# Kernel optimization log

Measured on AMD Instinct MI355X. Metric: run time of the kernel, lower is better.

## Reference

```python
import jax, jax.numpy as jnp
import numpy as np

C = 256
DEPTH = 4
GRIDS = [(128, 128), (128, 128), (128, 128)]
B = 2
N = 32768


def _ln_c(x, g, b):
    # LayerNorm over channel dim of [B, C, N] (myLayerNorm transposes to [B,N,C])
    m = x.mean(axis=1, keepdims=True)
    v = ((x - m) ** 2).mean(axis=1, keepdims=True)
    return (x - m) * jax.lax.rsqrt(v + 1e-5) * g[None, :, None] + b[None, :, None]


def _bn_train(x, g, b):
    # BatchNorm1d (training-mode batch stats) over [B, C, L]
    m = x.mean(axis=(0, 2), keepdims=True)
    v = ((x - m) ** 2).mean(axis=(0, 2), keepdims=True)
    return (x - m) * jax.lax.rsqrt(v + 1e-5) * g[None, :, None] + b[None, :, None]


def _dwconv3(x, w, b):
    # depthwise 3x3 conv, SAME padding; x [B,C,H,W], w [C,3,3]
    out = jax.lax.conv_general_dilated(x, w[:, None, :, :], (1, 1), 'SAME',
                                       feature_group_count=C,
                                       dimension_numbers=('NCHW', 'OIHW', 'NCHW'))
    return out + b[None, :, None, None]


def setup_inputs() -> dict:
    key = jax.random.key(0)
    ks = jax.random.split(key, 20)
    tokens = jax.random.normal(ks[0], (B, C, N), jnp.float32)
    hw = GRIDS[0][0] * GRIDS[0][1]
    cell_ind = jax.random.randint(ks[1], (B, 3, N), 0, hw)
    occupied_cell = jnp.ones((B, N), jnp.float32)

    def p(k, shape, scale=0.05):
        return scale * jax.random.normal(k, shape, jnp.float32)

    inp = dict(tokens=tokens, cell_ind=cell_ind, occupied_cell=occupied_cell)
    inp['smix_ln_g'] = 1.0 + p(ks[2], (DEPTH, C))
    inp['smix_ln_b'] = p(ks[3], (DEPTH, C))
    inp['ffn_w1'] = p(ks[4], (DEPTH, C, 3, 3), 0.2)
    inp['ffn_b1'] = p(ks[5], (DEPTH, C))
    inp['ffn_w2'] = p(ks[6], (DEPTH, C, 3, 3), 0.2)
    inp['ffn_b2'] = p(ks[7], (DEPTH, C))
    inp['att_scale'] = 1.0 + p(ks[8], (DEPTH, C))
    inp['att_bn_g'] = 1.0 + p(ks[9], (DEPTH, C))
    inp['att_bn_b'] = p(ks[10], (DEPTH, C))
    inp['cmix_ln_g'] = 1.0 + p(ks[11], (DEPTH, C))
    inp['cmix_ln_b'] = p(ks[12], (DEPTH, C))
    inp['cmix_w1'] = p(ks[13], (DEPTH, C, C), 1.0 / float(np.sqrt(C)))
    inp['cmix_b1'] = p(ks[14], (DEPTH, C))
    inp['cmix_w2'] = p(ks[15], (DEPTH, C, C), 1.0 / float(np.sqrt(C)))
    inp['cmix_b2'] = p(ks[16], (DEPTH, C))
    inp['cmix_scale'] = p(ks[17], (DEPTH, C), 0.1)
    return inp


def _forward(tokens, occupied_cell, cell_ind,
             smix_ln_g, smix_ln_b, ffn_w1, ffn_b1, ffn_w2, ffn_b2,
             att_scale, att_bn_g, att_bn_b,
             cmix_ln_g, cmix_ln_b, cmix_w1, cmix_b1, cmix_w2, cmix_b2, cmix_scale):
    Bx, Cx, Nx = tokens.shape
    bidx = jnp.arange(Bx)[:, None]
    # build_proj_matrix equivalent: per-point 1/(points-in-cell) weights + clamped indices
    sp = []
    for g in range(len(GRIDS)):
        HW = GRIDS[g][0] * GRIDS[g][1]
        ci = jnp.clip(cell_ind[:, g], 0, HW - 1)
        # inflate^T @ occupied: per-cell occupied count (occupied^2 per point)
        counts = jnp.zeros((Bx, HW), tokens.dtype).at[bidx, ci].add(occupied_cell * occupied_cell)
        # inflate @ counts: per-point count of points sharing its cell
        npp = occupied_cell * jnp.take_along_axis(counts, ci, axis=1)
        sp.append((ci, occupied_cell / (npp + 1e-6)))
    skip = [jnp.zeros(GRIDS[g], tokens.dtype) for g in range(len(GRIDS))]
    for d in range(DEPTH):
        g = d % len(GRIDS)
        H, W = GRIDS[g]
        HW = H * W
        ci, wpt = sp[g]
        # --- SpatialMix ---
        r = _ln_c(tokens, smix_ln_g[d], smix_ln_b[d]) * wpt[:, None, :]
        grid = jnp.zeros((Bx, Cx, HW), tokens.dtype).at[
            jnp.arange(Bx)[:, None, None], jnp.arange(Cx)[None, :, None], ci[:, None, :]].add(r)
        grid = grid.reshape(Bx, Cx, H, W) + skip[g]
        plane = _dwconv3(jax.nn.relu(_dwconv3(grid, ffn_w1[d], ffn_b1[d])), ffn_w2[d], ffn_b2[d])
        rflat = plane.reshape(Bx, Cx, HW)
        att = jax.nn.sigmoid(_bn_train(rflat * att_scale[d][None, :, None], att_bn_g[d], att_bn_b[d]))
        rflat = att * rflat
        r = jnp.take_along_axis(rflat, jnp.broadcast_to(ci[:, None, :], (Bx, Cx, Nx)), axis=2)
        tokens = tokens + r
        skip[g] = plane
        # --- ChannelMix ---
        h = _ln_c(tokens, cmix_ln_g[d], cmix_ln_b[d])
        h = jnp.einsum('oc,bcn->bon', cmix_w1[d], h) + cmix_b1[d][None, :, None]
        h = jnp.einsum('oc,bcn->bon', cmix_w2[d], jax.nn.relu(h)) + cmix_b2[d][None, :, None]
        tokens = tokens + h * cmix_scale[d][None, :, None]
    return tokens


def reference(tokens, cell_ind, occupied_cell,
              smix_ln_g, smix_ln_b, ffn_w1, ffn_b1, ffn_w2, ffn_b2,
              att_scale, att_bn_g, att_bn_b,
              cmix_ln_g, cmix_ln_b, cmix_w1, cmix_b1, cmix_w2, cmix_b2, cmix_scale):
    return _forward(tokens, occupied_cell, cell_ind,
                    smix_ln_g, smix_ln_b, ffn_w1, ffn_b1, ffn_w2, ffn_b2,
                    att_scale, att_bn_g, att_bn_b,
                    cmix_ln_g, cmix_ln_b, cmix_w1, cmix_b1, cmix_w2, cmix_b2, cmix_scale)
```

## Files before the change

kernel.cpp:

```cpp
#include <hip/hip_runtime.h>
#include <hip/hip_bf16.h>
#include <hip/hip_fp16.h>

#define Cc 256
#define Nn 32768
#define HWc 16384
#define Bb 2

typedef float floatx4 __attribute__((ext_vector_type(4)));
typedef short bf16x8 __attribute__((ext_vector_type(8)));
typedef unsigned short ushort8v __attribute__((ext_vector_type(8)));
typedef unsigned short ushort4v __attribute__((ext_vector_type(4)));

__device__ __forceinline__ unsigned short f2b(float f){
    unsigned u = __float_as_uint(f);
    u += 0x7fff + ((u >> 16) & 1);
    return (unsigned short)(u >> 16);
}
__device__ __forceinline__ float b2f(unsigned short h){
    return __uint_as_float(((unsigned)h) << 16);
}
__device__ __forceinline__ unsigned short f2h(float f){
    return __half_as_ushort(__float2half(f));
}
__device__ __forceinline__ float h2f(unsigned short h){
    return __half2float(__ushort_as_half(h));
}

__global__ __launch_bounds__(256) void k_count(const int* __restrict__ ci,
                                               const float* __restrict__ occ,
                                               float* __restrict__ fcounts,
                                               int* __restrict__ icounts){
    int idx = blockIdx.x*256 + threadIdx.x;
    if (idx >= Bb*3*Nn) return;
    int n = idx & (Nn-1);
    int bg = idx >> 15;
    int b = bg / 3;
    int cell = min(max(ci[idx], 0), HWc-1);
    float o = occ[(b<<15) + n];
    atomicAdd(&fcounts[(bg<<14) + cell], o*o);
    atomicAdd(&icounts[(bg<<14) + cell], 1);
}

__global__ __launch_bounds__(256) void k_wpt(const int* __restrict__ ci,
                                             const float* __restrict__ occ,
                                             const float* __restrict__ fcounts,
                                             float* __restrict__ wpt){
    int idx = blockIdx.x*256 + threadIdx.x;
    if (idx >= Bb*3*Nn) return;
    int n = idx & (Nn-1);
    int bg = idx >> 15;
    int b = bg / 3;
    int cell = min(max(ci[idx], 0), HWc-1);
    float o = occ[(b<<15) + n];
    float cnt = fcounts[(bg<<14) + cell];
    wpt[idx] = o / (o*cnt + 1e-6f);
}

__global__ __launch_bounds__(256) void k_scan(const int* __restrict__ ic,
                                              int* __restrict__ starts,
                                              int* __restrict__ cursor){
    __shared__ int part[256];
    int bg = blockIdx.x;
    int t = threadIdx.x;
    const int* cs = ic + (bg << 14);
    int base = t * 64;
    int s = 0;
    for (int i = 0; i < 64; ++i) s += cs[base + i];
    part[t] = s;
    __syncthreads();
    for (int off = 1; off < 256; off <<= 1){
        int v = (t >= off) ? part[t - off] : 0;
        __syncthreads();
        part[t] += v;
        __syncthreads();
    }
    int run = (t == 0) ? 0 : part[t - 1];
    int* st = starts + bg * (HWc + 1);
    int* cu = cursor + (bg << 14);
    for (int i = 0; i < 64; ++i){
        st[base + i] = run;
        cu[base + i] = run;
        run += cs[base + i];
    }
    if (t == 255) st[HWc] = run;
}

__global__ __launch_bounds__(256) void k_fill(const int* __restrict__ ci,
                                              int* __restrict__ cursor,
                                              int* __restrict__ plist){
    int idx = blockIdx.x*256 + threadIdx.x;
    if (idx >= Bb*3*Nn) return;
    int n = idx & (Nn-1);
    int bg = idx >> 15;
    int cell = min(max(ci[idx], 0), HWc-1);
    int pos = atomicAdd(&cursor[(bg<<14) + cell], 1);
    plist[(bg<<15) + pos] = n;
}

__global__ __launch_bounds__(256) void k_wcvt(const float* __restrict__ w1,
                                              const float* __restrict__ w2,
                                              unsigned short* __restrict__ W1b,
                                              unsigned short* __restrict__ W2b){
    int idx = blockIdx.x*256 + threadIdx.x;
    if (idx >= 4*Cc*Cc) return;
    W1b[idx] = f2b(w1[idx]);
    W2b[idx] = f2b(w2[idx]);
}

__global__ __launch_bounds__(256) void k1a_ln(const float* __restrict__ tok,
                                              const float* __restrict__ wpt,
                                              const float* __restrict__ lng,
                                              const float* __restrict__ lnb,
                                              unsigned short* __restrict__ rbuf, int g){
    __shared__ float lg[Cc], lb[Cc];
    int t = threadIdx.x;
    lg[t] = lng[t];
    lb[t] = lnb[t];
    __syncthreads();
    int b = blockIdx.x >> 7;
    int p = ((blockIdx.x & 127) << 8) + t;
    const float* tb = tok + ((size_t)b << 8)*Nn + p;
    float sum = 0.f, sq = 0.f;
    for (int c = 0; c < Cc; ++c){
        float x = tb[(size_t)c << 15];
        sum += x; sq += x*x;
    }
    float m = sum * (1.f/256.f);
    float v = sq * (1.f/256.f) - m*m;
    float r = rsqrtf(fmaxf(v, 0.f) + 1e-5f);
    float wv = wpt[(b*3 + g)*Nn + p];
    unsigned short* rb = rbuf + ((size_t)((b << 15) + p) << 8);
    for (int c0 = 0; c0 < Cc; c0 += 8){
        ushort8v u;
        #pragma unroll
        for (int j = 0; j < 8; ++j){
            int c = c0 + j;
            float x = tb[(size_t)c << 15];
            float h = ((x - m)*r*lg[c] + lb[c]) * wv;
            u[j] = f2h(h);
        }
        *(ushort8v*)(rb + c0) = u;
    }
}

__global__ __launch_bounds__(256) void k1b_gather(const unsigned short* __restrict__ rbuf,
                                                  const int* __restrict__ starts,
                                                  const int* __restrict__ plist,
                                                  unsigned short* __restrict__ grid, int g){
    int t = threadIdx.x;
    int bi = blockIdx.x;
    int b = bi >> 10;
    int cell0 = (bi & 1023) << 4;
    int bg = b*3 + g;
    const int* st = starts + bg*(HWc + 1) + cell0;
    const int* pl = plist + (bg << 15);
    const unsigned short* rb = rbuf + (((size_t)b << 15) << 8);
    float acc[16];
    int s0 = st[0];
    #pragma unroll
    for (int q = 0; q < 16; ++q){
        int s1 = st[q + 1];
        float a = 0.f;
        for (int j = s0; j < s1; ++j){
            int p = pl[j];
            a += h2f(rb[((size_t)p << 8) + t]);
        }
        acc[q] = a;
        s0 = s1;
    }
    unsigned short* go = grid + ((size_t)((b << 8) + t))*HWc + cell0;
    #pragma unroll
    for (int q = 0; q < 16; q += 8){
        ushort8v u;
        #pragma unroll
        for (int j = 0; j < 8; ++j) u[j] = f2h(acc[q+j]);
        *(ushort8v*)(go + q) = u;
    }
}

__global__ __launch_bounds__(256) void k2_conv(const unsigned short* __restrict__ grid,
                                               const unsigned short* __restrict__ skip,
                                               unsigned short* __restrict__ plane,
                                               const float* __restrict__ w1, const float* __restrict__ b1,
                                               const float* __restrict__ w2, const float* __restrict__ b2,
                                               const float* __restrict__ asc,
                                               float* __restrict__ bnS, float* __restrict__ bnQ,
                                               int useskip){
    __shared__ float it[36*132];
    __shared__ float mid[34*132];
    int tid = threadIdx.x;
    int bi = blockIdx.x;
    int rt = bi & 3;
    int bc = bi >> 2;
    int c = bc & 255;
    int r0 = rt << 5;
    const unsigned short* src = grid + (size_t)bc*HWc;
    const unsigned short* sk  = skip + (size_t)bc*HWc;
    for (int i = tid; i < 36*132; i += 256){
        int r = i / 132, cc = i - r*132;
        int gy = r0 - 2 + r, gx = cc - 2;
        float v = 0.f;
        if ((unsigned)gy < 128u && (unsigned)gx < 128u){
            int o = (gy << 7) + gx;
            v = h2f(src[o]);
            if (useskip) v += h2f(sk[o]);
        }
        it[i] = v;
    }
    float a1[9], a2[9];
    #pragma unroll
    for (int j = 0; j < 9; ++j){ a1[j] = w1[c*9+j]; a2[j] = w2[c*9+j]; }
    float bb1 = b1[c], bb2 = b2[c], sc = asc[c];
    __syncthreads();
    for (int i = tid; i < 34*130; i += 256){
        int r = i / 130, cc = i - r*130;
        int y = r0 - 1 + r, x = cc - 1;
        float v = 0.f;
        if ((unsigned)y < 128u && (unsigned)x < 128u){
            float s = 0.f;
            #pragma unroll
            for (int j = 0; j < 9; ++j) s += a1[j] * it[(r + j/3)*132 + cc + (j%3)];
            v = fmaxf(s + bb1, 0.f);
        }
        mid[r*132 + cc] = v;
    }
    __syncthreads();
    float ps = 0.f, pq = 0.f;
    unsigned short* dst = plane + (size_t)bc*HWc;
    for (int i = tid; i < 32*128; i += 256){
        int yy = i >> 7, x = i & 127;
        float s = 0.f;
        #pragma unroll
        for (int j = 0; j < 9; ++j) s += a2[j] * mid[(yy + j/3)*132 + x + (j%3)];
        float v = s + bb2;
        dst[((r0 + yy) << 7) + x] = f2h(v);
        float t = v * sc;
        ps += t; pq += t*t;
    }
    __syncthreads();
    it[tid] = ps; it[256 + tid] = pq;
    __syncthreads();
    for (int s2 = 128; s2 > 0; s2 >>= 1){
        if (tid < s2){ it[tid] += it[tid+s2]; it[256+tid] += it[256+tid+s2]; }
        __syncthreads();
    }
    if (tid == 0){
        atomicAdd(&bnS[c], it[0]);
        atomicAdd(&bnQ[c], it[256]);
    }
}

__global__ __launch_bounds__(256) void k2b_bn(const float* __restrict__ bnS, const float* __restrict__ bnQ,
                                              const float* __restrict__ asc,
                                              const float* __restrict__ bng, const float* __restrict__ bnb,
                                              float* __restrict__ P, float* __restrict__ Q){
    int c = threadIdx.x;
    float mean = bnS[c] * (1.f/32768.f);
    float var  = bnQ[c] * (1.f/32768.f) - mean*mean;
    float inv  = rsqrtf(fmaxf(var, 0.f) + 1e-5f) * bng[c];
    P[c] = asc[c] * inv;
    Q[c] = bnb[c] - mean * inv;
}

__global__ __launch_bounds__(256) void k3t_att_t(const unsigned short* __restrict__ plane,
                                                 const float* __restrict__ P, const float* __restrict__ Q,
                                                 unsigned short* __restrict__ attp){
    __shared__ float t[32*33];
    int tid = threadIdx.x;
    int tx = tid & 31, ty = tid >> 5;
    int bi = blockIdx.x;
    int ht = bi & 511;
    int ct = (bi >> 9) & 7;
    int b  = bi >> 12;
    int c0 = ct << 5, h0 = ht << 5;
    for (int r = ty; r < 32; r += 8){
        int c = c0 + r;
        float v = h2f(plane[(((size_t)b << 8) + c)*HWc + h0 + tx]);
        float s = 1.f / (1.f + __expf(-(P[c]*v + Q[c])));
        t[r*33 + tx] = s * v;
    }
    __syncthreads();
    for (int r = ty; r < 32; r += 8){
        attp[(((size_t)b << 14) + h0 + r)*Cc + c0 + tx] = f2h(t[tx*33 + r]);
    }
}

__global__ __launch_bounds__(512, 4) void k4_cmix(const float* __restrict__ tsrc, int tin_nc,
                                               float* __restrict__ tdst, int tout_nc,
                                               const unsigned short* __restrict__ attp,
                                               const int* __restrict__ ci,
                                               const unsigned short* __restrict__ W1,
                                               const unsigned short* __restrict__ W2,
                                               const float* __restrict__ lng, const float* __restrict__ lnb,
                                               const float* __restrict__ b1, const float* __restrict__ b2,
                                               const float* __restrict__ csc,
                                               const float* __restrict__ lng2, const float* __restrict__ lnb2,
                                               const float* __restrict__ wptb,
                                               unsigned short* __restrict__ rbufn,
                                               int g, int g2, int donext){
    __shared__ __align__(16) unsigned short hs[64*264];
    __shared__ float reds[512], redq[512];
    __shared__ float m_s[64], r_s[64];
    __shared__ int cell_s[64];
    __shared__ float lng_s[Cc], lnb_s[Cc], b1_s[Cc], b2s_s[Cc], cs_s[Cc], g2g_s[Cc], g2b_s[Cc];

    int tid = threadIdx.x;
    int bi = blockIdx.x;
    int b = bi >> 9;
    int p0 = (bi & 511) << 6;

    if (tid < 256){
        lng_s[tid] = lng[tid];
        lnb_s[tid] = lnb[tid];
        b1_s[tid]  = b1[tid];
        float cv = csc[tid];
        cs_s[tid]  = cv;
        b2s_s[tid] = b2[tid] * cv;
        g2g_s[tid] = lng2[tid];
        g2b_s[tid] = lnb2[tid];
    }
    if (tid < 64){
        int cc = ci[(b*3 + g)*Nn + p0 + tid];
        cell_s[tid] = min(max(cc, 0), HWc-1);
    }
    __syncthreads();

    int p  = tid & 63;
    int cg = tid >> 6;
    int c0 = cg << 5;

    const unsigned short* ar = attp + ((size_t)((b << 14) + cell_s[p]))*Cc + c0;
    ushort8v rr[4];
    #pragma unroll
    for (int j = 0; j < 4; ++j) rr[j] = *(const ushort8v*)(ar + 8*j);

    float vreg[32];
    float sum = 0.f, sq = 0.f;
    if (tin_nc){
        const floatx4* tn4 = (const floatx4*)(tsrc + ((((size_t)(b << 15)) + p0 + p) << 8) + c0);
        #pragma unroll
        for (int j = 0; j < 8; ++j){
            floatx4 f = tn4[j];
            #pragma unroll
            for (int e = 0; e < 4; ++e){
                int k = j*4 + e;
                float v = f[e] + h2f(rr[k >> 3][k & 7]);
                vreg[k] = v; sum += v; sq += v*v;
            }
        }
    } else {
        const float* tb = tsrc + ((size_t)b << 8)*Nn + p0 + p;
        #pragma unroll
        for (int k = 0; k < 32; ++k){
            float v = tb[(size_t)(c0 + k) << 15] + h2f(rr[k >> 3][k & 7]);
            vreg[k] = v; sum += v; sq += v*v;
        }
    }
    reds[tid] = sum; redq[tid] = sq;
    __syncthreads();
    if (tid < 64){
        float s = 0.f, q = 0.f;
        #pragma unroll
        for (int j = 0; j < 8; ++j){ s += reds[j*64 + tid]; q += redq[j*64 + tid]; }
        float m = s * (1.f/256.f);
        float var = q * (1.f/256.f) - m*m;
        m_s[tid] = m;
        r_s[tid] = rsqrtf(fmaxf(var, 0.f) + 1e-5f);
    }
    __syncthreads();
    float mp = m_s[p], rp = r_s[p];
    unsigned short* hrow = &hs[p*264 + c0];
    #pragma unroll
    for (int j = 0; j < 4; ++j){
        ushort8v u;
        #pragma unroll
        for (int e = 0; e < 8; ++e){
            int k = j*8 + e, c = c0 + k;
            u[e] = f2b((vreg[k] - mp)*rp*lng_s[c] + lnb_s[c]);
        }
        *(ushort8v*)(hrow + 8*j) = u;
    }
    __syncthreads();

    int lane = tid & 63;
    int w = tid >> 6;
    int l15 = lane & 15;
    int q4 = lane >> 4;
    floatx4 acc[2][4];
    #pragma unroll
    for (int mi = 0; mi < 2; ++mi)
        #pragma unroll
        for (int ni = 0; ni < 4; ++ni)
            acc[mi][ni] = (floatx4){0.f, 0.f, 0.f, 0.f};

    #pragma unroll
    for (int kk = 0; kk < 8; ++kk){
        int k0 = kk*32 + q4*8;
        bf16x8 bfr[4];
        #pragma unroll
        for (int ni = 0; ni < 4; ++ni)
            bfr[ni] = *(const bf16x8*)&hs[(ni*16 + l15)*264 + k0];
        #pragma unroll
        for (int mi = 0; mi < 2; ++mi){
            bf16x8 af = *(const bf16x8*)&W1[(size_t)(w*32 + mi*16 + l15)*Cc + k0];
            #pragma unroll
            for (int ni = 0; ni < 4; ++ni)
                acc[mi][ni] = __builtin_amdgcn_mfma_f32_16x16x32_bf16(af, bfr[ni], acc[mi][ni], 0, 0, 0);
        }
    }
    __syncthreads();
    #pragma unroll
    for (int mi = 0; mi < 2; ++mi)
        #pragma unroll
        for (int ni = 0; ni < 4; ++ni){
            int m0 = w*32 + mi*16 + q4*4;
            int nn = ni*16 + l15;
            ushort4v u;
            #pragma unroll
            for (int r = 0; r < 4; ++r)
                u[r] = f2b(fmaxf(acc[mi][ni][r] + b1_s[m0 + r], 0.f));
            *(ushort4v*)&hs[nn*264 + m0] = u;
        }
    __syncthreads();

    #pragma unroll
    for (int mi = 0; mi < 2; ++mi)
        #pragma unroll
        for (int ni = 0; ni < 4; ++ni)
            acc[mi][ni] = (floatx4){0.f, 0.f, 0.f, 0.f};
    #pragma unroll
    for (int kk = 0; kk < 8; ++kk){
        int k0 = kk*32 + q4*8;
        bf16x8 bfr[4];
        #pragma unroll
        for (int ni = 0; ni < 4; ++ni)
            bfr[ni] = *(const bf16x8*)&hs[(ni*16 + l15)*264 + k0];
        #pragma unroll
        for (int mi = 0; mi < 2; ++mi){
            bf16x8 af = *(const bf16x8*)&W2[(size_t)(w*32 + mi*16 + l15)*Cc + k0];
            #pragma unroll
            for (int ni = 0; ni < 4; ++ni)
                acc[mi][ni] = __builtin_amdgcn_mfma_f32_16x16x32_bf16(af, bfr[ni], acc[mi][ni], 0, 0, 0);
        }
    }
    __syncthreads();
    #pragma unroll
    for (int mi = 0; mi < 2; ++mi)
        #pragma unroll
        for (int ni = 0; ni < 4; ++ni){
            int m0 = w*32 + mi*16 + q4*4;
            int nn = ni*16 + l15;
            ushort4v u;
            #pragma unroll
            for (int r = 0; r < 4; ++r)
                u[r] = f2b(acc[mi][ni][r]*cs_s[m0 + r] + b2s_s[m0 + r]);
            *(ushort4v*)&hs[nn*264 + m0] = u;
        }
    __syncthreads();

    float sum2 = 0.f, sq2 = 0.f;
    if (tout_nc){
        float* tn = tdst + ((((size_t)(b << 15)) + p0 + p) << 8) + c0;
        #pragma unroll
        for (int j = 0; j < 4; ++j){
            ushort8v u = *(const ushort8v*)(hrow + 8*j);
            floatx4 fa, fb;
            #pragma unroll
            for (int e = 0; e < 4; ++e){
                int k = j*8 + e;
                float v = vreg[k] + b2f(u[e]);
                vreg[k] = v; fa[e] = v; sum2 += v; sq2 += v*v;
            }
            #pragma unroll
            for (int e = 4; e < 8; ++e){
                int k = j*8 + e;
                float v = vreg[k] + b2f(u[e]);
                vreg[k] = v; fb[e-4] = v; sum2 += v; sq2 += v*v;
            }
            *(floatx4*)(tn + 8*j) = fa;
            *(floatx4*)(tn + 8*j + 4) = fb;
        }
    } else {
        float* ob = tdst + ((size_t)b << 8)*Nn + p0 + p;
        #pragma unroll
        for (int j = 0; j < 4; ++j){
            ushort8v u = *(const ushort8v*)(hrow + 8*j);
            #pragma unroll
            for (int e = 0; e < 8; ++e){
                int k = j*8 + e, c = c0 + k;
                float v = vreg[k] + b2f(u[e]);
                vreg[k] = v;
                ob[(size_t)c << 15] = v;
                sum2 += v; sq2 += v*v;
            }
        }
    }
    if (donext){
        reds[tid] = sum2; redq[tid] = sq2;
        __syncthreads();
        if (tid < 64){
            float s = 0.f, q = 0.f;
            #pragma unroll
            for (int j = 0; j < 8; ++j){ s += reds[j*64 + tid]; q += redq[j*64 + tid]; }
            float m = s * (1.f/256.f);
            float var = q * (1.f/256.f) - m*m;
            m_s[tid] = m;
            r_s[tid] = rsqrtf(fmaxf(var, 0.f) + 1e-5f);
        }
        __syncthreads();
        float m2 = m_s[p], rr2 = r_s[p];
        float wv2 = wptb[(b*3 + g2)*Nn + p0 + p];
        unsigned short* rb = rbufn + ((size_t)((b << 15) + p0 + p))*Cc + c0;
        #pragma unroll
        for (int j = 0; j < 4; ++j){
            ushort8v u;
            #pragma unroll
            for (int e = 0; e < 8; ++e){
                int k = j*8 + e, c = c0 + k;
                u[e] = f2h(((vreg[k] - m2)*rr2*g2g_s[c] + g2b_s[c]) * wv2);
            }
            *(ushort8v*)(rb + 8*j) = u;
        }
    }
}

extern "C" void kernel_launch(void* const* d_in, const int* in_sizes, int n_in,
                              void* d_out, int out_size, void* d_ws, size_t ws_size,
                              hipStream_t stream){
    (void)in_sizes; (void)n_in; (void)out_size;
    const float* tokens  = (const float*)d_in[0];
    const int*   cellind = (const int*)d_in[1];
    const float* occ     = (const float*)d_in[2];
    const float* smix_g  = (const float*)d_in[3];
    const float* smix_b  = (const float*)d_in[4];
    const float* ffn_w1  = (const float*)d_in[5];
    const float* ffn_b1  = (const float*)d_in[6];
    const float* ffn_w2  = (const float*)d_in[7];
    const float* ffn_b2  = (const float*)d_in[8];
    const float* att_sc  = (const float*)d_in[9];
    const float* bn_g    = (const float*)d_in[10];
    const float* bn_b    = (const float*)d_in[11];
    const float* cm_g    = (const float*)d_in[12];
    const float* cm_b    = (const float*)d_in[13];
    const float* cw1     = (const float*)d_in[14];
    const float* cb1     = (const float*)d_in[15];
    const float* cw2     = (const float*)d_in[16];
    const float* cb2     = (const float*)d_in[17];
    const float* cscale  = (const float*)d_in[18];
    float* out = (float*)d_out;
    char* w = (char*)d_ws;

    const size_t HGRID_BYTES = (size_t)Bb*Cc*HWc*2;
    unsigned short* grid_h  = (unsigned short*)(w);
    unsigned short* attp_h  = grid_h;
    unsigned short* planeA  = (unsigned short*)(w + HGRID_BYTES);
    unsigned short* planeB  = (unsigned short*)(w + 2*HGRID_BYTES);
    unsigned short* rbuf    = (unsigned short*)(w + 3*HGRID_BYTES);
    size_t o = 3*HGRID_BYTES + (size_t)Bb*Nn*Cc*2;
    float* fcounts = (float*)(w + o); o += (size_t)Bb*3*HWc*4;
    int*   icounts = (int*)(w + o);   o += (size_t)Bb*3*HWc*4;
    float* wptb   = (float*)(w + o); o += (size_t)Bb*3*Nn*4;
    float* bnS    = (float*)(w + o);
    float* bnQ    = bnS + 256;
    float* Pb     = bnS + 512;
    float* Qb     = bnS + 768;
    o += 4096;
    unsigned short* W1b = (unsigned short*)(w + o);
    unsigned short* W2b = W1b + 4*Cc*Cc;
    o += (size_t)2*4*Cc*Cc*2;
    int* startsb  = (int*)(w + o); o += (size_t)Bb*3*(HWc+1)*4;
    int* cursors  = (int*)(w + o); o += (size_t)Bb*3*HWc*4;
    int* plistb   = (int*)(w + o); o += (size_t)Bb*3*Nn*4;
    o = (o + 255) & ~(size_t)255;
    float* tnc    = (float*)(w + o);
    size_t needed = o + (size_t)Bb*Nn*Cc*4;
    int nc_ok = (ws_size >= needed) ? 1 : 0;

    hipMemsetAsync(fcounts, 0, (size_t)2*Bb*3*HWc*4, stream);
    k_count<<<(Bb*3*Nn)/256, 256, 0, stream>>>(cellind, occ, fcounts, icounts);
    k_wpt<<<(Bb*3*Nn)/256, 256, 0, stream>>>(cellind, occ, fcounts, wptb);
    k_scan<<<Bb*3, 256, 0, stream>>>(icounts, startsb, cursors);
    k_fill<<<(Bb*3*Nn)/256, 256, 0, stream>>>(cellind, cursors, plistb);
    k_wcvt<<<(4*Cc*Cc)/256, 256, 0, stream>>>(cw1, cw2, W1b, W2b);

    k1a_ln<<<Bb*(Nn/256), 256, 0, stream>>>(tokens, wptb, smix_g, smix_b, rbuf, 0);

    for (int d = 0; d < 4; ++d){
        int g = d % 3;
        int g2 = (d + 1) % 3;
        int donext = (d < 3) ? 1 : 0;
        int useskip = (d == 3) ? 1 : 0;
        unsigned short* plane = (d == 0) ? planeA : planeB;
        int dn = (d + 1 < 4) ? d + 1 : d;

        const float* tsrc; int tin_nc;
        float* tdst; int tout_nc;
        if (nc_ok){
            tsrc = (d == 0) ? tokens : tnc;  tin_nc  = (d == 0) ? 0 : 1;
            tdst = (d == 3) ? out : tnc;     tout_nc = (d == 3) ? 0 : 1;
        } else {
            tsrc = (d == 0) ? tokens : out;  tin_nc  = 0;
            tdst = out;                      tout_nc = 0;
        }

        hipMemsetAsync(bnS, 0, 2048, stream);

        k1b_gather<<<Bb*(HWc/16), 256, 0, stream>>>(rbuf, startsb, plistb, grid_h, g);
        k2_conv<<<Bb*Cc*4, 256, 0, stream>>>(grid_h, planeA, plane,
                                             ffn_w1 + d*Cc*9, ffn_b1 + d*Cc,
                                             ffn_w2 + d*Cc*9, ffn_b2 + d*Cc,
                                             att_sc + d*Cc, bnS, bnQ, useskip);
        k2b_bn<<<1, 256, 0, stream>>>(bnS, bnQ, att_sc + d*Cc, bn_g + d*Cc, bn_b + d*Cc, Pb, Qb);
        k3t_att_t<<<Bb*8*512, 256, 0, stream>>>(plane, Pb, Qb, attp_h);
        k4_cmix<<<Bb*(Nn/64), 512, 0, stream>>>(tsrc, tin_nc, tdst, tout_nc, attp_h, cellind,
                                                W1b + (size_t)d*Cc*Cc, W2b + (size_t)d*Cc*Cc,
                                                cm_g + d*Cc, cm_b + d*Cc,
                                                cb1 + d*Cc, cb2 + d*Cc, cscale + d*Cc,
                                                smix_g + dn*Cc, smix_b + dn*Cc, wptb,
                                                rbuf, g, g2, donext);
    }
}
```

Measured before the change: 798.2 us.

## Restage gather via shared memory, fuse BN finalize into attention, trim cmix shared state

The gather kernel now handles 32 cells per block, stages the point list and cell starts in shared memory, and transposes accumulators through LDS so each thread writes contiguous 16-byte runs. The standalone BN-finalize kernel is removed and its per-channel scale/offset computation is folded into the attention transpose kernel, saving a launch. The channel-mix kernel drops most of its shared parameter arrays and reads biases, scales and LN params directly as vector global loads, reducing LDS footprint and one barrier, possibly raising occupancy. The trade-offs are redundant BN math per attention block and a larger gather block footprint.

```diff
diff --git a/kernel.cpp b/kernel.cpp
--- a/kernel.cpp
+++ b/kernel.cpp
@@ -148,34 +148,50 @@
                                                   const int* __restrict__ starts,
                                                   const int* __restrict__ plist,
                                                   unsigned short* __restrict__ grid, int g){
+    __shared__ float acc[256*33];
+    __shared__ int pl_s[1024];
+    __shared__ int st_s[33];
     int t = threadIdx.x;
     int bi = blockIdx.x;
-    int b = bi >> 10;
-    int cell0 = (bi & 1023) << 4;
+    int b = bi >> 9;
+    int cell0 = (bi & 511) << 5;
     int bg = b*3 + g;
     const int* st = starts + bg*(HWc + 1) + cell0;
-    const int* pl = plist + (bg << 15);
-    const unsigned short* rb = rbuf + (((size_t)b << 15) << 8);
-    float acc[16];
-    int s0 = st[0];
-    #pragma unroll
-    for (int q = 0; q < 16; ++q){
-        int s1 = st[q + 1];
+    if (t < 33) st_s[t] = st[t];
+    __syncthreads();
+    int base = st_s[0];
+    int npts = st_s[32] - base;
+    const int* pl = plist + (bg << 15) + base;
+    bool staged = (npts <= 1024);
+    if (staged){
+        for (int i = t; i < npts; i += 256) pl_s[i] = pl[i];
+    }
+    __syncthreads();
+    const unsigned short* rb = rbuf + (((size_t)b << 15) << 8) + t;
+    for (int c = 0; c < 32; ++c){
+        int s0 = st_s[c] - base, s1 = st_s[c+1] - base;
         float a = 0.f;
-        for (int j = s0; j < s1; ++j){
-            int p = pl[j];
-            a += h2f(rb[((size_t)p << 8) + t]);
-        }
-        acc[q] = a;
-        s0 = s1;
-    }
-    unsigned short* go = grid + ((size_t)((b << 8) + t))*HWc + cell0;
-    #pragma unroll
-    for (int q = 0; q < 16; q += 8){
+        if (staged){
+            for (int j = s0; j < s1; ++j)
+                a += h2f(rb[(size_t)pl_s[j] << 8]);
+        } else {
+            for (int j = s0; j < s1; ++j)
+                a += h2f(rb[(size_t)pl[j] << 8]);
+        }
+        acc[t*33 + c] = a;
+    }
+    __syncthreads();
+    unsigned short* go = grid + (((size_t)b << 8))*HWc + cell0;
+    int ch4 = t & 3;
+    int cr  = t >> 2;
+    #pragma unroll
+    for (int rr = 0; rr < 4; ++rr){
+        int c = rr*64 + cr;
         ushort8v u;
         #pragma unroll
-        for (int j = 0; j < 8; ++j) u[j] = f2h(acc[q+j]);
-        *(ushort8v*)(go + q) = u;
+        for (int e = 0; e < 8; ++e)
+            u[e] = f2h(acc[c*33 + ch4*8 + e]);
+        *(ushort8v*)(go + (size_t)c*HWc + ch4*8) = u;
     }
 }
 
@@ -251,22 +267,13 @@
     }
 }
 
-__global__ __launch_bounds__(256) void k2b_bn(const float* __restrict__ bnS, const float* __restrict__ bnQ,
-                                              const float* __restrict__ asc,
-                                              const float* __restrict__ bng, const float* __restrict__ bnb,
-                                              float* __restrict__ P, float* __restrict__ Q){
-    int c = threadIdx.x;
-    float mean = bnS[c] * (1.f/32768.f);
-    float var  = bnQ[c] * (1.f/32768.f) - mean*mean;
-    float inv  = rsqrtf(fmaxf(var, 0.f) + 1e-5f) * bng[c];
-    P[c] = asc[c] * inv;
-    Q[c] = bnb[c] - mean * inv;
-}
-
 __global__ __launch_bounds__(256) void k3t_att_t(const unsigned short* __restrict__ plane,
-                                                 const float* __restrict__ P, const float* __restrict__ Q,
+                                                 const float* __restrict__ bnS, const float* __restrict__ bnQ,
+                                                 const float* __restrict__ asc,
+                                                 const float* __restrict__ bng, const float* __restrict__ bnb,
                                                  unsigned short* __restrict__ attp){
     __shared__ float t[32*33];
+    __shared__ float P_s[32], Q_s[32];
     int tid = threadIdx.x;
     int tx = tid & 31, ty = tid >> 5;
     int bi = blockIdx.x;
@@ -274,10 +281,19 @@
     int ct = (bi >> 9) & 7;
     int b  = bi >> 12;
     int c0 = ct << 5, h0 = ht << 5;
+    if (tid < 32){
+        int c = c0 + tid;
+        float mean = bnS[c] * (1.f/32768.f);
+        float var  = bnQ[c] * (1.f/32768.f) - mean*mean;
+        float inv  = rsqrtf(fmaxf(var, 0.f) + 1e-5f) * bng[c];
+        P_s[tid] = asc[c] * inv;
+        Q_s[tid] = bnb[c] - mean * inv;
+    }
+    __syncthreads();
     for (int r = ty; r < 32; r += 8){
         int c = c0 + r;
         float v = h2f(plane[(((size_t)b << 8) + c)*HWc + h0 + tx]);
-        float s = 1.f / (1.f + __expf(-(P[c]*v + Q[c])));
+        float s = 1.f / (1.f + __expf(-(P_s[r]*v + Q_s[r])));
         t[r*33 + tx] = s * v;
     }
     __syncthreads();
@@ -302,8 +318,7 @@
     __shared__ __align__(16) unsigned short hs[64*264];
     __shared__ float reds[512], redq[512];
     __shared__ float m_s[64], r_s[64];
-    __shared__ int cell_s[64];
-    __shared__ float lng_s[Cc], lnb_s[Cc], b1_s[Cc], b2s_s[Cc], cs_s[Cc], g2g_s[Cc], g2b_s[Cc];
+    __shared__ float lng_s[Cc], lnb_s[Cc];
 
     int tid = threadIdx.x;
     int bi = blockIdx.x;
@@ -313,24 +328,16 @@
     if (tid < 256){
         lng_s[tid] = lng[tid];
         lnb_s[tid] = lnb[tid];
-        b1_s[tid]  = b1[tid];
-        float cv = csc[tid];
-        cs_s[tid]  = cv;
-        b2s_s[tid] = b2[tid] * cv;
-        g2g_s[tid] = lng2[tid];
-        g2b_s[tid] = lnb2[tid];
-    }
-    if (tid < 64){
-        int cc = ci[(b*3 + g)*Nn + p0 + tid];
-        cell_s[tid] = min(max(cc, 0), HWc-1);
-    }
-    __syncthreads();
+    }
 
     int p  = tid & 63;
     int cg = tid >> 6;
     int c0 = cg << 5;
 
-    const unsigned short* ar = attp + ((size_t)((b << 14) + cell_s[p]))*Cc + c0;
+    int cell = ci[(b*3 + g)*Nn + p0 + p];
+    cell = min(max(cell, 0), HWc-1);
+
+    const unsigned short* ar = attp + ((size_t)((b << 14) + cell))*Cc + c0;
     ushort8v rr[4];
     #pragma unroll
     for (int j = 0; j < 4; ++j) rr[j] = *(const ushort8v*)(ar + 8*j);
@@ -357,6 +364,7 @@
             vreg[k] = v; sum += v; sq += v*v;
         }
     }
+    __syncthreads();
     reds[tid] = sum; redq[tid] = sq;
     __syncthreads();
     if (tid < 64){
@@ -411,17 +419,19 @@
     }
     __syncthreads();
     #pragma unroll
-    for (int mi = 0; mi < 2; ++mi)
+    for (int mi = 0; mi < 2; ++mi){
+        int m0 = w*32 + mi*16 + q4*4;
+        floatx4 b14 = *(const floatx4*)&b1[m0];
         #pragma unroll
         for (int ni = 0; ni < 4; ++ni){
-            int m0 = w*32 + mi*16 + q4*4;
             int nn = ni*16 + l15;
             ushort4v u;
             #pragma unroll
             for (int r = 0; r < 4; ++r)
-                u[r] = f2b(fmaxf(acc[mi][ni][r] + b1_s[m0 + r], 0.f));
+                u[r] = f2b(fmaxf(acc[mi][ni][r] + b14[r], 0.f));
             *(ushort4v*)&hs[nn*264 + m0] = u;
         }
+    }
     __syncthreads();
 
     #pragma unroll
@@ -446,17 +456,20 @@
     }
     __syncthreads();
     #pragma unroll
-    for (int mi = 0; mi < 2; ++mi)
+    for (int mi = 0; mi < 2; ++mi){
+        int m0 = w*32 + mi*16 + q4*4;
+        floatx4 cs4 = *(const floatx4*)&csc[m0];
+        floatx4 b24 = *(const floatx4*)&b2[m0];
         #pragma unroll
         for (int ni = 0; ni < 4; ++ni){
-            int m0 = w*32 + mi*16 + q4*4;
             int nn = ni*16 + l15;
             ushort4v u;
             #pragma unroll
             for (int r = 0; r < 4; ++r)
-                u[r] = f2b(acc[mi][ni][r]*cs_s[m0 + r] + b2s_s[m0 + r]);
+                u[r] = f2b((acc[mi][ni][r] + b24[r]) * cs4[r]);
             *(ushort4v*)&hs[nn*264 + m0] = u;
         }
+    }
     __syncthreads();
 
     float sum2 = 0.f, sq2 = 0.f;
@@ -514,11 +527,20 @@
         unsigned short* rb = rbufn + ((size_t)((b << 15) + p0 + p))*Cc + c0;
         #pragma unroll
         for (int j = 0; j < 4; ++j){
+            floatx4 ga0 = *(const floatx4*)&lng2[c0 + j*8];
+            floatx4 ga1 = *(const floatx4*)&lng2[c0 + j*8 + 4];
+            floatx4 gb0 = *(const floatx4*)&lnb2[c0 + j*8];
+            floatx4 gb1 = *(const floatx4*)&lnb2[c0 + j*8 + 4];
             ushort8v u;
             #pragma unroll
-            for (int e = 0; e < 8; ++e){
-                int k = j*8 + e, c = c0 + k;
-                u[e] = f2h(((vreg[k] - m2)*rr2*g2g_s[c] + g2b_s[c]) * wv2);
+            for (int e = 0; e < 4; ++e){
+                int k = j*8 + e;
+                u[e] = f2h(((vreg[k] - m2)*rr2*ga0[e] + gb0[e]) * wv2);
+            }
+            #pragma unroll
+            for (int e = 4; e < 8; ++e){
+                int k = j*8 + e;
+                u[e] = f2h(((vreg[k] - m2)*rr2*ga1[e-4] + gb1[e-4]) * wv2);
             }
             *(ushort8v*)(rb + 8*j) = u;
         }
@@ -563,8 +585,6 @@
     float* wptb   = (float*)(w + o); o += (size_t)Bb*3*Nn*4;
     float* bnS    = (float*)(w + o);
     float* bnQ    = bnS + 256;
-    float* Pb     = bnS + 512;
-    float* Qb     = bnS + 768;
     o += 4096;
     unsigned short* W1b = (unsigned short*)(w + o);
     unsigned short* W2b = W1b + 4*Cc*Cc;
@@ -606,13 +626,13 @@
 
         hipMemsetAsync(bnS, 0, 2048, stream);
 
-        k1b_gather<<<Bb*(HWc/16), 256, 0, stream>>>(rbuf, startsb, plistb, grid_h, g);
+        k1b_gather<<<Bb*(HWc/32), 256, 0, stream>>>(rbuf, startsb, plistb, grid_h, g);
         k2_conv<<<Bb*Cc*4, 256, 0, stream>>>(grid_h, planeA, plane,
                                              ffn_w1 + d*Cc*9, ffn_b1 + d*Cc,
                                              ffn_w2 + d*Cc*9, ffn_b2 + d*Cc,
                                              att_sc + d*Cc, bnS, bnQ, useskip);
-        k2b_bn<<<1, 256, 0, stream>>>(bnS, bnQ, att_sc + d*Cc, bn_g + d*Cc, bn_b + d*Cc, Pb, Qb);
-        k3t_att_t<<<Bb*8*512, 256, 0, stream>>>(plane, Pb, Qb, attp_h);
+        k3t_att_t<<<Bb*8*512, 256, 0, stream>>>(plane, bnS, bnQ, att_sc + d*Cc,
+                                                bn_g + d*Cc, bn_b + d*Cc, attp_h);
         k4_cmix<<<Bb*(Nn/64), 512, 0, stream>>>(tsrc, tin_nc, tdst, tout_nc, attp_h, cellind,
                                                 W1b + (size_t)d*Cc*Cc, W2b + (size_t)d*Cc*Cc,
                                                 cm_g + d*Cc, cm_b + d*Cc,
```

New measurement: 846.4 us. 6.0% more time.
